# Kernel tuning notes

Hardware: AMD Instinct MI355X
Metric: run time of the kernel (lower is better)

The kernel has to match this reference:

```python
import jax, jax.numpy as jnp
import numpy as np

D_MODEL = 2048
NUM_HEADS = 16
D_K = D_MODEL // NUM_HEADS  # 128
MAX_SEQ_LEN = 4096
THETA = 10000.0
BATCH = 2
SEQ = 2048


def _trunc_normal(key, shape, std):
    # approximate trunc_normal_(mean=0, std, a=-3std, b=3std)
    return jnp.clip(jax.random.normal(key, shape) * std, -3 * std, 3 * std)


def setup_inputs() -> dict:
    key = jax.random.key(0)
    k0, k1, k2, k3, k4 = jax.random.split(key, 5)
    std = 2.0 / (D_MODEL + D_MODEL) ** 0.5
    in_features = jax.random.normal(k0, (BATCH, SEQ, D_MODEL), dtype=jnp.float32)
    token_positions = jnp.arange(SEQ, dtype=jnp.int64 if jax.config.jax_enable_x64 else jnp.int32)
    wq = _trunc_normal(k1, (D_MODEL, D_MODEL), std)
    wk = _trunc_normal(k2, (D_MODEL, D_MODEL), std)
    wv = _trunc_normal(k3, (D_MODEL, D_MODEL), std)
    wo = _trunc_normal(k4, (D_MODEL, D_MODEL), std)
    return {"in_features": in_features, "token_positions": token_positions,
            "wq": wq, "wk": wk, "wv": wv, "wo": wo}


def _rope(x, token_positions):
    # x: [b, h, s, d_k]; token_positions: [s]
    freqs = 1.0 / THETA ** (jnp.arange(0, D_K, 2, dtype=jnp.float32) / D_K)  # [d_k/2]
    angles = token_positions.astype(jnp.float32)[:, None] * freqs[None, :]   # [s, d_k/2]
    sin = jnp.sin(angles)
    cos = jnp.cos(angles)
    x1 = x[..., ::2]
    x2 = x[..., 1::2]
    rot = jnp.stack([x1 * cos - x2 * sin, x1 * sin + x2 * cos], axis=-1)  # [b,h,s,d_k/2,2]
    return rot.reshape(x.shape)


def reference(in_features, token_positions, wq, wk, wv, wo):
    b, s, _ = in_features.shape
    # projections: weight is [d_out, d_in]
    q = jnp.einsum('oi,bsi->bso', wq, in_features)
    k = jnp.einsum('oi,bsi->bso', wk, in_features)
    v = jnp.einsum('oi,bsi->bso', wv, in_features)
    # split heads: [b, s, h*d] -> [b, h, s, d]
    def split(t):
        return t.reshape(b, s, NUM_HEADS, D_K).transpose(0, 2, 1, 3)
    q, k, v = split(q), split(k), split(v)
    q = _rope(q, token_positions)
    k = _rope(k, token_positions)
    scores = jnp.einsum('bhqd,bhkd->bhqk', q, k) / jnp.sqrt(jnp.float32(D_K))
    causal = jnp.tril(jnp.ones((s, s), dtype=bool))
    scores = jnp.where(causal, scores, -jnp.inf)
    attn = jax.nn.softmax(scores, axis=-1)
    out = jnp.einsum('bhqk,bhkd->bhqd', attn, v)
    out = out.transpose(0, 2, 1, 3).reshape(b, s, D_MODEL)
    return jnp.einsum('oi,bsi->bso', wo, out)
```

## Files before the change

### kernel.cpp

```cpp
#include <hip/hip_runtime.h>
#include <cstdint>

typedef unsigned short u16;
typedef __attribute__((ext_vector_type(8))) short short8;
typedef __attribute__((ext_vector_type(4))) float f32x4;
typedef __attribute__((ext_vector_type(16))) float f32x16;
typedef __attribute__((ext_vector_type(2))) unsigned int uint2v;

#define D_MODEL 2048
#define NHEAD   16
#define DK      128
#define SEQQ    2048
#define BATCH   2
#define MTOT    (BATCH*SEQQ)

#define FENCE() asm volatile("" ::: "memory")
#define BARRIER() do { FENCE(); __builtin_amdgcn_s_barrier(); FENCE(); } while (0)

__device__ __forceinline__ u16 f2b(float f) {
  union { float f; uint32_t u; } c; c.f = f;
  uint32_t u = c.u;
  u += 0x7fffu + ((u >> 16) & 1u);
  return (u16)(u >> 16);
}
__device__ __forceinline__ float b2f(u16 h) {
  union { uint32_t u; float f; } c; c.u = ((uint32_t)h) << 16;
  return c.f;
}

__device__ __forceinline__ void gload_lds16(const void* g, void* l) {
  __builtin_amdgcn_global_load_lds(
      (const __attribute__((address_space(1))) void*)(uintptr_t)g,
      (__attribute__((address_space(3))) void*)(uint32_t)(uintptr_t)l,
      16, 0, 0);
}

template<int WO>
__global__ __launch_bounds__(256) void cvt_allk(const float* __restrict__ x,
                                                const float* __restrict__ wq,
                                                const float* __restrict__ wk,
                                                const float* __restrict__ wv,
                                                const float* __restrict__ wo,
                                                const int* __restrict__ pos,
                                                u16* __restrict__ Xb,
                                                u16* __restrict__ Wqkv,
                                                u16* __restrict__ Wob,
                                                float2* __restrict__ Tab) {
  int i = blockIdx.x * 256 + threadIdx.x;
  constexpr int NX = 2097152;
  constexpr int NW = 1048576;
  constexpr int WEND = NX + 3 * NW;
  constexpr int WOEND = WO ? WEND + NW : WEND;
  if (i < WOEND) {
    const float* src; u16* dst; int j;
    if (i < NX) { src = x; dst = Xb; j = i; }
    else if (i < WEND) {
      int t = i - NX;
      int w = t >> 20; j = t & (NW - 1);
      src = (w == 0) ? wq : (w == 1) ? wk : wv;
      dst = Wqkv + (size_t)w * 4194304;
    } else { src = wo; dst = Wob; j = i - WEND; }
    float4 v = ((const float4*)src)[j];
    union { u16 s[4]; uint64_t q; } o;
    o.s[0] = f2b(v.x); o.s[1] = f2b(v.y); o.s[2] = f2b(v.z); o.s[3] = f2b(v.w);
    ((uint64_t*)dst)[j] = o.q;
  } else {
    int idx = i - WOEND;
    int s = idx >> 6, j = idx & 63;
    float ang = (float)pos[s] * exp2f((float)j * -0.20762050593046014f);
    float sn, cs;
    sincosf(ang, &sn, &cs);
    Tab[idx] = make_float2(cs, sn);
  }
}

__global__ __launch_bounds__(256) void cvt_wo(const float* __restrict__ wo,
                                              u16* __restrict__ Wob) {
  int i = blockIdx.x * 256 + threadIdx.x;
  float4 v = ((const float4*)wo)[i];
  union { u16 s[4]; uint64_t q; } o;
  o.s[0] = f2b(v.x); o.s[1] = f2b(v.y); o.s[2] = f2b(v.z); o.s[3] = f2b(v.w);
  ((uint64_t*)Wob)[i] = o.q;
}

template<int MF, int NF, int MODE, int MAP>
__global__ __launch_bounds__(512) void gemmT(const u16* __restrict__ A,
                                             const u16* __restrict__ B,
                                             u16* __restrict__ Cq, u16* __restrict__ Ck,
                                             u16* __restrict__ Vt, float* __restrict__ Cf,
                                             const float2* __restrict__ Tab,
                                             int nbm, int cpx) {
  constexpr int BM = MF * 32;
  constexpr int BN = NF * 64;
  constexpr int AG = BM / 64;
  constexpr int BG = NF;
  __shared__ __align__(16) u16 As[2][BM * 64];
  __shared__ __align__(16) u16 Bs[2][BN * 64];
  const int tid = threadIdx.x;
  const int wave = tid >> 6, lane = tid & 63;
  const int l15 = lane & 15, l4 = lane >> 4;
  const int wr = wave >> 2, wc = wave & 3;
  int bm, bn;
  if (MAP == 1) {
    const int xcd = (int)blockIdx.x & 7;
    const int loc = (int)blockIdx.x >> 3;
    bm = ((loc >> 5) << 3) + (loc & 7);
    bn = xcd * 4 + ((loc >> 3) & 3);
  } else {
    const int wg = ((int)blockIdx.x & 7) * cpx + ((int)blockIdx.x >> 3);
    bm = wg % nbm; bn = wg / nbm;
  }
  const int row0 = bm * BM, col0 = bn * BN;

  const u16* asrc[AG]; const u16* bsrc[BG];
  {
    const int r = tid >> 3, c8 = tid & 7;
#pragma unroll
    for (int g = 0; g < AG; ++g) {
      int row = g * 64 + r;
      asrc[g] = A + (size_t)(row0 + row) * 2048 + ((c8 ^ (row & 7)) << 3);
    }
#pragma unroll
    for (int g = 0; g < BG; ++g) {
      int row = g * 64 + r;
      bsrc[g] = B + (size_t)(col0 + row) * 2048 + ((c8 ^ (row & 7)) << 3);
    }
  }
  const int ldst = tid * 8;

  int aoff[MF][2], boff[NF][2];
#pragma unroll
  for (int m = 0; m < MF; ++m) {
    int row = wr * (MF * 16) + m * 16 + l15;
#pragma unroll
    for (int ks = 0; ks < 2; ++ks)
      aoff[m][ks] = row * 64 + (((ks * 4 + l4) ^ (l15 & 7)) << 3);
  }
#pragma unroll
  for (int n = 0; n < NF; ++n) {
    int row = wc * (NF * 16) + n * 16 + l15;
#pragma unroll
    for (int ks = 0; ks < 2; ++ks)
      boff[n][ks] = row * 64 + (((ks * 4 + l4) ^ (l15 & 7)) << 3);
  }

  f32x4 acc[MF][NF] = {};

#pragma unroll
  for (int g = 0; g < AG; ++g) gload_lds16(asrc[g], &As[0][g * 4096 + ldst]);
#pragma unroll
  for (int g = 0; g < BG; ++g) gload_lds16(bsrc[g], &Bs[0][g * 4096 + ldst]);

  for (int t = 0; t < 32; ++t) {
    const int buf = t & 1;
    __syncthreads();
    if (t + 1 < 32) {
#pragma unroll
      for (int g = 0; g < AG; ++g) gload_lds16(asrc[g] + ((t + 1) << 6), &As[buf ^ 1][g * 4096 + ldst]);
#pragma unroll
      for (int g = 0; g < BG; ++g) gload_lds16(bsrc[g] + ((t + 1) << 6), &Bs[buf ^ 1][g * 4096 + ldst]);
    }
    short8 bfr[NF][2], afr[MF][2];
#pragma unroll
    for (int n = 0; n < NF; ++n)
#pragma unroll
      for (int ks = 0; ks < 2; ++ks)
        bfr[n][ks] = *(const short8*)&Bs[buf][boff[n][ks]];
#pragma unroll
    for (int m = 0; m < MF; ++m)
#pragma unroll
      for (int ks = 0; ks < 2; ++ks)
        afr[m][ks] = *(const short8*)&As[buf][aoff[m][ks]];
    __builtin_amdgcn_s_setprio(1);
#pragma unroll
    for (int ks = 0; ks < 2; ++ks)
#pragma unroll
      for (int n = 0; n < NF; ++n)
#pragma unroll
        for (int m = 0; m < MF; ++m)
          acc[m][n] = __builtin_amdgcn_mfma_f32_16x16x32_bf16(afr[m][ks], bfr[n][ks], acc[m][n], 0, 0, 0);
    __builtin_amdgcn_s_setprio(0);
  }

#pragma unroll
  for (int m = 0; m < MF; ++m) {
    const int row = row0 + wr * (MF * 16) + m * 16 + l4 * 4;
#pragma unroll
    for (int n = 0; n < NF; ++n) {
      const int col = col0 + wc * (NF * 16) + n * 16 + l15;
      if (MODE == 1) {
#pragma unroll
        for (int r = 0; r < 4; ++r)
          Cf[(size_t)(row + r) * 2048 + col] = acc[m][n][r];
      } else {
        const int region = col >> 11;
        const int col2 = col & 2047;
        if (region < 2) {
          u16* Cx = region ? Ck : Cq;
          const float2* tp = Tab + (size_t)(row & 2047) * 64 + ((col2 & 127) >> 1);
          const float sg = (col2 & 1) ? 1.0f : -1.0f;
#pragma unroll
          for (int r = 0; r < 4; ++r) {
            float v = acc[m][n][r];
            float p = __int_as_float(
                __builtin_amdgcn_mov_dpp(__float_as_int(v), 0xB1, 0xF, 0xF, true));
            float2 cs = tp[(size_t)r * 64];
            Cx[(size_t)(row + r) * 2048 + col2] = f2b(fmaf(sg * p, cs.y, v * cs.x));
          }
        } else {
          union { u16 h4[4]; uint64_t q; } pk;
#pragma unroll
          for (int r = 0; r < 4; ++r) pk.h4[r] = f2b(acc[m][n][r]);
          const int bb = row >> 11, ss = row & 2047;
          const int hh = col2 >> 7, dd = col2 & 127;
          *(uint64_t*)&Vt[((size_t)((bb << 4) + hh) * 128 + dd) * 2048 + ss] = pk.q;
        }
      }
    }
  }
}

__global__ __launch_bounds__(256) void attn_fwd(const u16* __restrict__ Q,
                                                const u16* __restrict__ Kg,
                                                const u16* __restrict__ Vt,
                                                u16* __restrict__ O) {
  __shared__ __align__(16) u16 Klds[2][64 * 128];
  __shared__ __align__(16) u16 Vlds[2][128 * 64];
  const int tid = threadIdx.x, wave = tid >> 6, lane = tid & 63;
  const int l31 = lane & 31, l5 = lane >> 5;
  const int bh = blockIdx.x;
  const int bxr = 15 - (int)blockIdx.y;
  const int b = bh >> 4, h = bh & 15;
  const int q0 = bxr * 128, qw = q0 + wave * 32;
  const float qscale = 0.1275174470974136f;

  short8 bq[8];
  {
    const u16* Qp = Q + (size_t)(b * SEQQ + qw + l31) * D_MODEL + h * DK + l5 * 8;
#pragma unroll
    for (int dt = 0; dt < 8; ++dt) {
      short8 raw = *(const short8*)(Qp + dt * 16);
#pragma unroll
      for (int j = 0; j < 8; ++j) raw[j] = (short)f2b(b2f((u16)raw[j]) * qscale);
      bq[dt] = raw;
    }
  }

  f32x16 facc[4] = {};
  float lpart = 0.f;

  const u16* Kbase = Kg + (size_t)b * SEQQ * D_MODEL + h * DK;
  const u16* Vbase = Vt + (size_t)bh * DK * SEQQ;
  const u16* ksrc[4]; const u16* vsrc[4];
#pragma unroll
  for (int g = 0; g < 4; ++g) {
    int kr = g * 16 + (tid >> 4);
    int kc = ((tid & 15) * 8) ^ ((kr & 7) << 3);
    ksrc[g] = Kbase + (size_t)kr * D_MODEL + kc;
    int vr = g * 32 + (tid >> 3);
    int vc = ((tid & 7) * 8) ^ ((vr & 7) << 3);
    vsrc[g] = Vbase + (size_t)vr * SEQQ + vc;
  }
  const int dstoff = tid * 8;
  const int nkt = 2 * (bxr + 1);

#pragma unroll
  for (int g = 0; g < 4; ++g) { gload_lds16(ksrc[g], &Klds[0][g * 2048 + dstoff]); ksrc[g] += (size_t)64 * D_MODEL; }
#pragma unroll
  for (int g = 0; g < 4; ++g) { gload_lds16(vsrc[g], &Vlds[0][g * 2048 + dstoff]); vsrc[g] += 64; }

  for (int kt = 0; kt < nkt; ++kt) {
    const int k0 = kt * 64, cur = kt & 1;
    __syncthreads();
    if (kt + 1 < nkt) {
#pragma unroll
      for (int g = 0; g < 4; ++g) { gload_lds16(ksrc[g], &Klds[cur ^ 1][g * 2048 + dstoff]); ksrc[g] += (size_t)64 * D_MODEL; }
#pragma unroll
      for (int g = 0; g < 4; ++g) { gload_lds16(vsrc[g], &Vlds[cur ^ 1][g * 2048 + dstoff]); vsrc[g] += 64; }
    }
    if (k0 > qw + 31) continue;

    const u16* Kl = Klds[cur];
    const u16* Vl = Vlds[cur];

    f32x16 st0 = {}, st1 = {}, st0b = {}, st1b = {};
    __builtin_amdgcn_s_setprio(1);
#pragma unroll
    for (int dtp = 0; dtp < 4; ++dtp) {
      const int dt0 = 2 * dtp, dt1 = 2 * dtp + 1;
      const int ch0 = ((2 * dt0 + l5) ^ (l31 & 7)) * 8;
      const int ch1 = ((2 * dt1 + l5) ^ (l31 & 7)) * 8;
      short8 ak00 = *(const short8*)&Kl[l31 * 128 + ch0];
      short8 ak10 = *(const short8*)&Kl[(32 + l31) * 128 + ch0];
      short8 ak01 = *(const short8*)&Kl[l31 * 128 + ch1];
      short8 ak11 = *(const short8*)&Kl[(32 + l31) * 128 + ch1];
      st0  = __builtin_amdgcn_mfma_f32_32x32x16_bf16(ak00, bq[dt0], st0, 0, 0, 0);
      st1  = __builtin_amdgcn_mfma_f32_32x32x16_bf16(ak10, bq[dt0], st1, 0, 0, 0);
      st0b = __builtin_amdgcn_mfma_f32_32x32x16_bf16(ak01, bq[dt1], st0b, 0, 0, 0);
      st1b = __builtin_amdgcn_mfma_f32_32x32x16_bf16(ak11, bq[dt1], st1b, 0, 0, 0);
    }
    __builtin_amdgcn_s_setprio(0);
    st0 += st0b;
    st1 += st1b;

    if (k0 + 63 > qw) {
      const int qm = qw + l31 - k0 - 4 * l5;
#pragma unroll
      for (int r = 0; r < 16; ++r) {
        const int kc0 = (r & 3) + 8 * (r >> 2);
        st0[r] = (kc0 > qm) ? -1e30f : st0[r];
        st1[r] = (kc0 + 32 > qm) ? -1e30f : st1[r];
      }
    }

    float psv[4] = {0.f, 0.f, 0.f, 0.f};
#pragma unroll
    for (int r = 0; r < 16; ++r) { float p = exp2f(st0[r]); st0[r] = p; psv[r & 3] += p; }
#pragma unroll
    for (int r = 0; r < 16; ++r) { float p = exp2f(st1[r]); st1[r] = p; psv[r & 3] += p; }
    lpart += (psv[0] + psv[1]) + (psv[2] + psv[3]);

    short8 pa[4];
#pragma unroll
    for (int ks2 = 0; ks2 < 2; ++ks2) {
#pragma unroll
      for (int t0 = 0; t0 < 2; ++t0) {
        uint32_t c0w0, c0w1, c1w0, c1w1;
        if (ks2 == 0) {
          asm("v_cvt_pk_bf16_f32 %0, %1, %2" : "=v"(c0w0) : "v"(st0[8 * t0 + 0]), "v"(st0[8 * t0 + 1]));
          asm("v_cvt_pk_bf16_f32 %0, %1, %2" : "=v"(c0w1) : "v"(st0[8 * t0 + 2]), "v"(st0[8 * t0 + 3]));
          asm("v_cvt_pk_bf16_f32 %0, %1, %2" : "=v"(c1w0) : "v"(st0[8 * t0 + 4]), "v"(st0[8 * t0 + 5]));
          asm("v_cvt_pk_bf16_f32 %0, %1, %2" : "=v"(c1w1) : "v"(st0[8 * t0 + 6]), "v"(st0[8 * t0 + 7]));
        } else {
          asm("v_cvt_pk_bf16_f32 %0, %1, %2" : "=v"(c0w0) : "v"(st1[8 * t0 + 0]), "v"(st1[8 * t0 + 1]));
          asm("v_cvt_pk_bf16_f32 %0, %1, %2" : "=v"(c0w1) : "v"(st1[8 * t0 + 2]), "v"(st1[8 * t0 + 3]));
          asm("v_cvt_pk_bf16_f32 %0, %1, %2" : "=v"(c1w0) : "v"(st1[8 * t0 + 4]), "v"(st1[8 * t0 + 5]));
          asm("v_cvt_pk_bf16_f32 %0, %1, %2" : "=v"(c1w1) : "v"(st1[8 * t0 + 6]), "v"(st1[8 * t0 + 7]));
        }
        uint2v s0 = __builtin_amdgcn_permlane32_swap(c0w0, c1w0, false, false);
        uint2v s1 = __builtin_amdgcn_permlane32_swap(c0w1, c1w1, false, false);
        union { uint32_t w[4]; short8 v; } u;
        u.w[0] = s0.x; u.w[1] = s1.x; u.w[2] = s0.y; u.w[3] = s1.y;
        pa[2 * ks2 + t0] = u.v;
      }
    }

    __builtin_amdgcn_s_setprio(1);
#pragma unroll
    for (int t = 0; t < 4; ++t) {
#pragma unroll
      for (int db = 0; db < 4; ++db) {
        const int row = 32 * db + l31;
        const int ch = ((2 * t + l5) ^ (l31 & 7)) * 8;
        short8 av = *(const short8*)&Vl[row * 64 + ch];
        facc[db] = __builtin_amdgcn_mfma_f32_32x32x16_bf16(av, pa[t], facc[db], 0, 0, 0);
      }
    }
    __builtin_amdgcn_s_setprio(0);
  }

  float inv;
  {
    uint2v sw = __builtin_amdgcn_permlane32_swap(__float_as_uint(lpart), __float_as_uint(lpart), false, false);
    inv = 1.0f / (__uint_as_float(sw.x) + __uint_as_float(sw.y));
  }
  u16* Op = O + (size_t)(b * SEQQ + qw + l31) * D_MODEL + h * DK;
#pragma unroll
  for (int db = 0; db < 4; ++db)
#pragma unroll
    for (int a = 0; a < 4; ++a) {
      union { u16 h4[4]; uint64_t q; } pk;
#pragma unroll
      for (int c = 0; c < 4; ++c) pk.h4[c] = f2b(facc[db][4 * a + c] * inv);
      *(uint64_t*)&Op[32 * db + 8 * a + 4 * l5] = pk.q;
    }
}

extern "C" void kernel_launch(void* const* d_in, const int* in_sizes, int n_in,
                              void* d_out, int out_size, void* d_ws, size_t ws_size,
                              hipStream_t stream) {
  const float* x   = (const float*)d_in[0];
  const int*   pos = (const int*)d_in[1];
  const float* wq  = (const float*)d_in[2];
  const float* wk  = (const float*)d_in[3];
  const float* wv  = (const float*)d_in[4];
  const float* wo  = (const float*)d_in[5];
  float* out = (float*)d_out;
  char* ws = (char*)d_ws;

  u16* Xb   = (u16*)(ws);
  u16* Wqkv = (u16*)(ws + (16u << 20));
  u16* Wob  = (u16*)(ws + (40u << 20));
  u16* Qb   = (u16*)(ws + (48u << 20));
  u16* Kb   = (u16*)(ws + (64u << 20));
  u16* Vt   = (u16*)(ws + (80u << 20));
  u16* AO   = Xb;

  const bool sep = (ws_size >= ((size_t)97 << 20));
  float2* Tab = sep ? (float2*)(ws + ((size_t)96 << 20))
                    : (float2*)(ws + (40u << 20));

  if (sep)
    cvt_allk<1><<<25088, 256, 0, stream>>>(x, wq, wk, wv, wo, pos, Xb, Wqkv, Wob, Tab);
  else
    cvt_allk<0><<<20992, 256, 0, stream>>>(x, wq, wk, wv, wo, pos, Xb, Wqkv, Wob, Tab);

  gemmT<4, 3, 0, 1><<<1024, 512, 0, stream>>>(Xb, Wqkv, Qb, Kb, Vt, nullptr, Tab, 32, 128);

  if (!sep)
    cvt_wo<<<4096, 256, 0, stream>>>(wo, Wob);

  attn_fwd<<<dim3(32, 16), 256, 0, stream>>>(Qb, Kb, Vt, AO);

  gemmT<4, 4, 1, 0><<<256, 512, 0, stream>>>(AO, Wob, nullptr, nullptr, nullptr, out, Tab, 32, 32);
}
```

Before: 239.3 us.

## Skip fully-masked key half on diagonal tiles and compute softmax denominator via MFMA

On the diagonal tile where the key block starts at the wave's first query row, the upper 32 keys are entirely masked, so the QK^T, exp, conversion and PV work for that half is skipped. The per-lane exp-sum and the permlane reduction are replaced by an extra MFMA against a vector of bf16 ones, which accumulates the row denominator from the same bf16 probabilities used for PV. This adds one MFMA per PV step and turns the PV loop into a runtime-bounded loop, which may hurt scheduling. The QK^T accumulation also drops its two-chain interleave and becomes one dependent chain per half.

```diff
diff --git a/kernel.cpp b/kernel.cpp
--- a/kernel.cpp
+++ b/kernel.cpp
@@ -246,8 +246,12 @@
     }
   }
 
+  short8 ones8;
+#pragma unroll
+  for (int j = 0; j < 8; ++j) ones8[j] = (short)0x3F80;
+
   f32x16 facc[4] = {};
-  float lpart = 0.f;
+  f32x16 dacc = {};
 
   const u16* Kbase = Kg + (size_t)b * SEQQ * D_MODEL + h * DK;
   const u16* Vbase = Vt + (size_t)bh * DK * SEQQ;
@@ -282,72 +286,81 @@
 
     const u16* Kl = Klds[cur];
     const u16* Vl = Vlds[cur];
-
-    f32x16 st0 = {}, st1 = {}, st0b = {}, st1b = {};
+    const bool do1 = (k0 != qw);
+
+    f32x16 st0 = {}, st1 = {};
     __builtin_amdgcn_s_setprio(1);
 #pragma unroll
-    for (int dtp = 0; dtp < 4; ++dtp) {
-      const int dt0 = 2 * dtp, dt1 = 2 * dtp + 1;
-      const int ch0 = ((2 * dt0 + l5) ^ (l31 & 7)) * 8;
-      const int ch1 = ((2 * dt1 + l5) ^ (l31 & 7)) * 8;
-      short8 ak00 = *(const short8*)&Kl[l31 * 128 + ch0];
-      short8 ak10 = *(const short8*)&Kl[(32 + l31) * 128 + ch0];
-      short8 ak01 = *(const short8*)&Kl[l31 * 128 + ch1];
-      short8 ak11 = *(const short8*)&Kl[(32 + l31) * 128 + ch1];
-      st0  = __builtin_amdgcn_mfma_f32_32x32x16_bf16(ak00, bq[dt0], st0, 0, 0, 0);
-      st1  = __builtin_amdgcn_mfma_f32_32x32x16_bf16(ak10, bq[dt0], st1, 0, 0, 0);
-      st0b = __builtin_amdgcn_mfma_f32_32x32x16_bf16(ak01, bq[dt1], st0b, 0, 0, 0);
-      st1b = __builtin_amdgcn_mfma_f32_32x32x16_bf16(ak11, bq[dt1], st1b, 0, 0, 0);
+    for (int dt = 0; dt < 8; ++dt) {
+      const int ch = ((2 * dt + l5) ^ (l31 & 7)) * 8;
+      short8 ak0 = *(const short8*)&Kl[l31 * 128 + ch];
+      st0 = __builtin_amdgcn_mfma_f32_32x32x16_bf16(ak0, bq[dt], st0, 0, 0, 0);
+    }
+    if (do1) {
+#pragma unroll
+      for (int dt = 0; dt < 8; ++dt) {
+        const int ch = ((2 * dt + l5) ^ (l31 & 7)) * 8;
+        short8 ak1 = *(const short8*)&Kl[(32 + l31) * 128 + ch];
+        st1 = __builtin_amdgcn_mfma_f32_32x32x16_bf16(ak1, bq[dt], st1, 0, 0, 0);
+      }
     }
     __builtin_amdgcn_s_setprio(0);
-    st0 += st0b;
-    st1 += st1b;
-
-    if (k0 + 63 > qw) {
-      const int qm = qw + l31 - k0 - 4 * l5;
+
+    const int qm = qw + l31 - k0 - 4 * l5;
+    if (!do1) {
 #pragma unroll
       for (int r = 0; r < 16; ++r) {
         const int kc0 = (r & 3) + 8 * (r >> 2);
         st0[r] = (kc0 > qm) ? -1e30f : st0[r];
+      }
+    } else if (k0 + 63 > qw) {
+#pragma unroll
+      for (int r = 0; r < 16; ++r) {
+        const int kc0 = (r & 3) + 8 * (r >> 2);
         st1[r] = (kc0 + 32 > qm) ? -1e30f : st1[r];
       }
     }
 
-    float psv[4] = {0.f, 0.f, 0.f, 0.f};
-#pragma unroll
-    for (int r = 0; r < 16; ++r) { float p = exp2f(st0[r]); st0[r] = p; psv[r & 3] += p; }
-#pragma unroll
-    for (int r = 0; r < 16; ++r) { float p = exp2f(st1[r]); st1[r] = p; psv[r & 3] += p; }
-    lpart += (psv[0] + psv[1]) + (psv[2] + psv[3]);
+#pragma unroll
+    for (int r = 0; r < 16; ++r) st0[r] = exp2f(st0[r]);
+    if (do1) {
+#pragma unroll
+      for (int r = 0; r < 16; ++r) st1[r] = exp2f(st1[r]);
+    }
 
     short8 pa[4];
 #pragma unroll
-    for (int ks2 = 0; ks2 < 2; ++ks2) {
+    for (int t0 = 0; t0 < 2; ++t0) {
+      uint32_t c0w0, c0w1, c1w0, c1w1;
+      asm("v_cvt_pk_bf16_f32 %0, %1, %2" : "=v"(c0w0) : "v"(st0[8 * t0 + 0]), "v"(st0[8 * t0 + 1]));
+      asm("v_cvt_pk_bf16_f32 %0, %1, %2" : "=v"(c0w1) : "v"(st0[8 * t0 + 2]), "v"(st0[8 * t0 + 3]));
+      asm("v_cvt_pk_bf16_f32 %0, %1, %2" : "=v"(c1w0) : "v"(st0[8 * t0 + 4]), "v"(st0[8 * t0 + 5]));
+      asm("v_cvt_pk_bf16_f32 %0, %1, %2" : "=v"(c1w1) : "v"(st0[8 * t0 + 6]), "v"(st0[8 * t0 + 7]));
+      uint2v s0 = __builtin_amdgcn_permlane32_swap(c0w0, c1w0, false, false);
+      uint2v s1 = __builtin_amdgcn_permlane32_swap(c0w1, c1w1, false, false);
+      union { uint32_t w[4]; short8 v; } u;
+      u.w[0] = s0.x; u.w[1] = s1.x; u.w[2] = s0.y; u.w[3] = s1.y;
+      pa[t0] = u.v;
+    }
+    if (do1) {
 #pragma unroll
       for (int t0 = 0; t0 < 2; ++t0) {
         uint32_t c0w0, c0w1, c1w0, c1w1;
-        if (ks2 == 0) {
-          asm("v_cvt_pk_bf16_f32 %0, %1, %2" : "=v"(c0w0) : "v"(st0[8 * t0 + 0]), "v"(st0[8 * t0 + 1]));
-          asm("v_cvt_pk_bf16_f32 %0, %1, %2" : "=v"(c0w1) : "v"(st0[8 * t0 + 2]), "v"(st0[8 * t0 + 3]));
-          asm("v_cvt_pk_bf16_f32 %0, %1, %2" : "=v"(c1w0) : "v"(st0[8 * t0 + 4]), "v"(st0[8 * t0 + 5]));
-          asm("v_cvt_pk_bf16_f32 %0, %1, %2" : "=v"(c1w1) : "v"(st0[8 * t0 + 6]), "v"(st0[8 * t0 + 7]));
-        } else {
-          asm("v_cvt_pk_bf16_f32 %0, %1, %2" : "=v"(c0w0) : "v"(st1[8 * t0 + 0]), "v"(st1[8 * t0 + 1]));
-          asm("v_cvt_pk_bf16_f32 %0, %1, %2" : "=v"(c0w1) : "v"(st1[8 * t0 + 2]), "v"(st1[8 * t0 + 3]));
-          asm("v_cvt_pk_bf16_f32 %0, %1, %2" : "=v"(c1w0) : "v"(st1[8 * t0 + 4]), "v"(st1[8 * t0 + 5]));
-          asm("v_cvt_pk_bf16_f32 %0, %1, %2" : "=v"(c1w1) : "v"(st1[8 * t0 + 6]), "v"(st1[8 * t0 + 7]));
-        }
+        asm("v_cvt_pk_bf16_f32 %0, %1, %2" : "=v"(c0w0) : "v"(st1[8 * t0 + 0]), "v"(st1[8 * t0 + 1]));
+        asm("v_cvt_pk_bf16_f32 %0, %1, %2" : "=v"(c0w1) : "v"(st1[8 * t0 + 2]), "v"(st1[8 * t0 + 3]));
+        asm("v_cvt_pk_bf16_f32 %0, %1, %2" : "=v"(c1w0) : "v"(st1[8 * t0 + 4]), "v"(st1[8 * t0 + 5]));
+        asm("v_cvt_pk_bf16_f32 %0, %1, %2" : "=v"(c1w1) : "v"(st1[8 * t0 + 6]), "v"(st1[8 * t0 + 7]));
         uint2v s0 = __builtin_amdgcn_permlane32_swap(c0w0, c1w0, false, false);
         uint2v s1 = __builtin_amdgcn_permlane32_swap(c0w1, c1w1, false, false);
         union { uint32_t w[4]; short8 v; } u;
         u.w[0] = s0.x; u.w[1] = s1.x; u.w[2] = s0.y; u.w[3] = s1.y;
-        pa[2 * ks2 + t0] = u.v;
-      }
-    }
-
+        pa[2 + t0] = u.v;
+      }
+    }
+
+    const int nt = do1 ? 4 : 2;
     __builtin_amdgcn_s_setprio(1);
-#pragma unroll
-    for (int t = 0; t < 4; ++t) {
+    for (int t = 0; t < nt; ++t) {
 #pragma unroll
       for (int db = 0; db < 4; ++db) {
         const int row = 32 * db + l31;
@@ -355,15 +368,12 @@
         short8 av = *(const short8*)&Vl[row * 64 + ch];
         facc[db] = __builtin_amdgcn_mfma_f32_32x32x16_bf16(av, pa[t], facc[db], 0, 0, 0);
       }
+      dacc = __builtin_amdgcn_mfma_f32_32x32x16_bf16(ones8, pa[t], dacc, 0, 0, 0);
     }
     __builtin_amdgcn_s_setprio(0);
   }
 
-  float inv;
-  {
-    uint2v sw = __builtin_amdgcn_permlane32_swap(__float_as_uint(lpart), __float_as_uint(lpart), false, false);
-    inv = 1.0f / (__uint_as_float(sw.x) + __uint_as_float(sw.y));
-  }
+  const float inv = 1.0f / dacc[0];
   u16* Op = O + (size_t)(b * SEQQ + qw + l31) * D_MODEL + h * DK;
 #pragma unroll
   for (int db = 0; db < 4; ++db)
```

Result: slower. 496.6 us (+107.6%).
